# Kernel tuning notes

Measured on AMD Instinct MI355X. Metric: run time of the kernel, lower is better.

The kernel has to match this reference:

```python
import jax, jax.numpy as jnp
import numpy as np

Y = 1      # init kwarg y
DIM = 2    # init kwarg dim


def setup_inputs() -> dict:
    key = jax.random.key(0)
    k1, k2, k3 = jax.random.split(key, 3)
    B, L = 16, 512
    H = 32
    x = jax.random.normal(k1, (B, L, L), dtype=jnp.float32)
    # xavier_uniform-like init for weights
    lim1 = np.sqrt(6.0 / (3 + H)).astype(np.float32)
    W1 = jax.random.uniform(k2, (H, 3), dtype=jnp.float32, minval=-lim1, maxval=lim1)
    b1 = jnp.zeros((H,), dtype=jnp.float32)
    lim2 = np.sqrt(6.0 / (H + 1)).astype(np.float32)
    W2 = jax.random.uniform(k3, (1, H), dtype=jnp.float32, minval=-lim2, maxval=lim2)
    b2 = jnp.zeros((1,), dtype=jnp.float32)
    return {"x": x, "W1": W1, "b1": b1, "W2": W2, "b2": b2}


def reference(x, W1, b1, W2, b2):
    # nearest-neighbor sum along both lattice dims
    x1 = (jnp.roll(x, 1, axis=1) + jnp.roll(x, -1, axis=1)
          + jnp.roll(x, 1, axis=2) + jnp.roll(x, -1, axis=2))
    # shifted-by-y neighbor sum along DIM
    sx = jnp.roll(x, Y, axis=DIM) + jnp.roll(x, -Y, axis=DIM)
    # per-site 3-feature vector: [x^2, x1*x, sx*x] -> (B, L, L, 3)
    inp = jnp.stack([x * x, x1 * x, sx * x], axis=-1)
    # tiny pointwise MLP 3 -> 32 -> 1
    h = jnp.tanh(jnp.einsum('blmf,hf->blmh', inp, W1) + b1)
    out = jnp.einsum('blmh,oh->blmo', h, W2)[..., 0] + b2[0]
    # sum over lattice sites -> per-config scalar (B,)
    return out.sum(axis=(1, 2))
```

## Files before the change

### kernel.cpp

```cpp
#include <hip/hip_runtime.h>

#define L 512
#define LMASK 511
#define HID 32

constexpr int THREADS        = 256;
constexpr int ROWS_PER_BLOCK = 4;
constexpr int BLOCKS_PER_B   = L / ROWS_PER_BLOCK;
constexpr int NTAB           = 4096;
constexpr int GT             = 5;
constexpr int NPAIR_E        = 6;

constexpr float MAGIC = 8388608.0f;
constexpr float BIASB = 8194.0f;

__global__ __launch_bounds__(THREADS)
void site_kernel(const float* __restrict__ x,
                 const float* __restrict__ W1,
                 const float* __restrict__ b1,
                 const float* __restrict__ W2,
                 float* __restrict__ partial) {
    __shared__ __align__(16) float tab_s[NTAB];
    __shared__ __align__(16) float zw_s[GT * 16];
    __shared__ __align__(16) float w2t_s[GT * 4];
    __shared__ __align__(16) float ew_s[NPAIR_E * 8];
    __shared__ __align__(8)  float ew2_s[NPAIR_E * 2];

    const int t = threadIdx.x;
    const float Ke = 2.8853900817779268f;

    if (t < HID) {
        if (t < 4 * GT) {
            const float K256 = 256.0f * Ke;
            const int g = t >> 2, q = t & 3;
            zw_s[g * 16 +  0 + q] = K256 * W1[t * 3 + 0];
            zw_s[g * 16 +  4 + q] = K256 * W1[t * 3 + 1];
            zw_s[g * 16 +  8 + q] = K256 * W1[t * 3 + 2];
            zw_s[g * 16 + 12 + q] = fmaf(K256, b1[t], BIASB + MAGIC);
            w2t_s[t] = -2.0f * W2[t];
        } else {
            const int e = t - 4 * GT, p = e >> 1, q = e & 1;
            ew_s[p * 8 + 0 + q] = Ke * W1[t * 3 + 0];
            ew_s[p * 8 + 2 + q] = Ke * W1[t * 3 + 1];
            ew_s[p * 8 + 4 + q] = Ke * W1[t * 3 + 2];
            ew_s[p * 8 + 6 + q] = Ke * b1[t];
            ew2_s[p * 2 + q]    = -2.0f * W2[t];
        }
    }
    for (int i = t; i < NTAB; i += THREADS) {
        const float zp = fmaf((float)i, 0.015625f, -32.001953125f);
        tab_s[i] = __builtin_amdgcn_rcpf(1.0f + __builtin_amdgcn_exp2f(zp));
    }
    __syncthreads();

    const int blk = blockIdx.x;
    const int b   = blk >> 7;
    const int i0  = (blk & (BLOCKS_PER_B - 1)) * ROWS_PER_BLOCK;
    const float* __restrict__ xb = x + (size_t)b * (L * L);

    float F0[8], F1[8], F2[8];
#pragma unroll
    for (int g = 0; g < 2; ++g) {
        const int j  = t + g * THREADS;
        const int jm = (j + LMASK) & LMASK, jp = (j + 1) & LMASK;

        float cc[6];
#pragma unroll
        for (int r = 0; r < 6; ++r) {
            const int i = (i0 + r - 1 + L) & LMASK;
            cc[r] = xb[i * L + j];
        }
#pragma unroll
        for (int s = 0; s < 4; ++s) {
            const int i   = i0 + s;
            const float lf = xb[i * L + jm];
            const float rg = xb[i * L + jp];
            const float c  = cc[s + 1];
            const float lr = lf + rg;
            const float x1 = lr + cc[s] + cc[s + 2];
            const int k = g * 4 + s;
            F0[k] = c * c;  F1[k] = x1 * c;  F2[k] = lr * c;
        }
    }

    float acc[8] = {0.f, 0.f, 0.f, 0.f, 0.f, 0.f, 0.f, 0.f};
    const char* __restrict__ tb = (const char*)tab_s;

    auto tgroup = [&](const int gq) {
        const float4 wa  = *(const float4*)&zw_s[gq * 16 + 0];
        const float4 wb  = *(const float4*)&zw_s[gq * 16 + 4];
        const float4 wc  = *(const float4*)&zw_s[gq * 16 + 8];
        const float4 w0  = *(const float4*)&zw_s[gq * 16 + 12];
        const float4 w2v = *(const float4*)&w2t_s[gq * 4];
#pragma unroll
        for (int q = 0; q < 4; ++q) {
            const float waq = ((const float*)&wa)[q];
            const float wbq = ((const float*)&wb)[q];
            const float wcq = ((const float*)&wc)[q];
            const float w0q = ((const float*)&w0)[q];
            const float w2q = ((const float*)&w2v)[q];
#pragma unroll
            for (int s = 0; s < 8; ++s) {
                const float uu = fmaf(F0[s], waq, fmaf(F1[s], wbq, fmaf(F2[s], wcq, w0q)));
                const int  off = __float_as_int(uu) & 0x3FFC;
                const float y  = *reinterpret_cast<const float*>(tb + off);
                acc[s] = fmaf(w2q, y, acc[s]);
            }
        }
    };
    auto epair = [&](const int p) {
        const float4 e0 = *(const float4*)&ew_s[p * 8 + 0];
        const float4 e1 = *(const float4*)&ew_s[p * 8 + 4];
        const float2 w2p = *(const float2*)&ew2_s[p * 2];
        const float wa0 = e0.x, wa1 = e0.y, wb0 = e0.z, wb1 = e0.w;
        const float wc0 = e1.x, wc1 = e1.y, w00 = e1.z, w01 = e1.w;
#pragma unroll
        for (int s = 0; s < 8; ++s) {
            const float z0 = fmaf(F0[s], wa0, fmaf(F1[s], wb0, fmaf(F2[s], wc0, w00)));
            const float z1 = fmaf(F0[s], wa1, fmaf(F1[s], wb1, fmaf(F2[s], wc1, w01)));
            const float d0 = 1.0f + __builtin_amdgcn_exp2f(z0);
            const float d1 = 1.0f + __builtin_amdgcn_exp2f(z1);
            const float nm = fmaf(w2p.x, d1, w2p.y * d0);
            const float rr = __builtin_amdgcn_rcpf(d0 * d1);
            acc[s] = fmaf(nm, rr, acc[s]);
        }
    };

    tgroup(0); epair(0);
    tgroup(1); epair(1);
    tgroup(2); epair(2);
    tgroup(3); epair(3);
    tgroup(4); epair(4); epair(5);

    float a = ((acc[0] + acc[1]) + (acc[2] + acc[3]))
            + ((acc[4] + acc[5]) + (acc[6] + acc[7]));
#pragma unroll
    for (int off = 32; off > 0; off >>= 1)
        a += __shfl_down(a, off, 64);

    __shared__ float wsum[THREADS / 64];
    const int wid = t >> 6, lane = t & 63;
    if (lane == 0) wsum[wid] = a;
    __syncthreads();
    if (t == 0)
        partial[blk] = (wsum[0] + wsum[1]) + (wsum[2] + wsum[3]);
}

__global__ __launch_bounds__(128)
void reduce_kernel(const float* __restrict__ partial,
                   const float* __restrict__ W2,
                   const float* __restrict__ b2,
                   float* __restrict__ out) {
    const int b = blockIdx.x, t = threadIdx.x;
    const float NS = (float)(L * L);

    float v = partial[b * BLOCKS_PER_B + t];
    if (t < HID) v += NS * W2[t];
    if (t == 0)  v += NS * b2[0];

#pragma unroll
    for (int off = 32; off > 0; off >>= 1)
        v += __shfl_down(v, off, 64);

    __shared__ float ws2[2];
    if ((t & 63) == 0) ws2[t >> 6] = v;
    __syncthreads();
    if (t == 0) out[b] = ws2[0] + ws2[1];
}

extern "C" void kernel_launch(void* const* d_in, const int* in_sizes, int n_in,
                              void* d_out, int out_size, void* d_ws, size_t ws_size,
                              hipStream_t stream) {
    const float* x  = (const float*)d_in[0];
    const float* W1 = (const float*)d_in[1];
    const float* b1 = (const float*)d_in[2];
    const float* W2 = (const float*)d_in[3];
    const float* b2 = (const float*)d_in[4];
    float* out      = (float*)d_out;
    float* partial  = (float*)d_ws;

    const int B = in_sizes[0] / (L * L);

    site_kernel<<<B * BLOCKS_PER_B, THREADS, 0, stream>>>(x, W1, b1, W2, partial);
    reduce_kernel<<<B, 128, 0, stream>>>(partial, W2, b2, out);
}
```

Baseline: 34.15 us.

## Halve rows per block and split table lookups into address/load/consume phases

Each block now covers 2 rows instead of 4, which doubles the grid to 4096 blocks, and the reduce kernel is widened to 256 threads to match. The table-lookup path is split into three steps: compute all 16 LDS offsets, issue all 16 LDS loads, run the exp-based pair evaluation, then consume the loaded values. This interleaves LDS latency with transcendental work. In exchange, every block still builds the 4096-entry sigmoid table, so twice as many blocks repeat that setup, and halo rows are reloaded more often.

```diff
diff --git a/kernel.cpp b/kernel.cpp
--- a/kernel.cpp
+++ b/kernel.cpp
@@ -5,7 +5,7 @@
 #define HID 32
 
 constexpr int THREADS        = 256;
-constexpr int ROWS_PER_BLOCK = 4;
+constexpr int ROWS_PER_BLOCK = 2;
 constexpr int BLOCKS_PER_B   = L / ROWS_PER_BLOCK;
 constexpr int NTAB           = 4096;
 constexpr int GT             = 5;
@@ -54,86 +54,100 @@
     __syncthreads();
 
     const int blk = blockIdx.x;
-    const int b   = blk >> 7;
+    const int b   = blk >> 8;
     const int i0  = (blk & (BLOCKS_PER_B - 1)) * ROWS_PER_BLOCK;
     const float* __restrict__ xb = x + (size_t)b * (L * L);
 
-    float F0[8], F1[8], F2[8];
+    float F0[4], F1[4], F2[4];
 #pragma unroll
     for (int g = 0; g < 2; ++g) {
         const int j  = t + g * THREADS;
         const int jm = (j + LMASK) & LMASK, jp = (j + 1) & LMASK;
 
-        float cc[6];
-#pragma unroll
-        for (int r = 0; r < 6; ++r) {
+        float cc[4];
+#pragma unroll
+        for (int r = 0; r < 4; ++r) {
             const int i = (i0 + r - 1 + L) & LMASK;
             cc[r] = xb[i * L + j];
         }
 #pragma unroll
-        for (int s = 0; s < 4; ++s) {
+        for (int s = 0; s < 2; ++s) {
             const int i   = i0 + s;
             const float lf = xb[i * L + jm];
             const float rg = xb[i * L + jp];
             const float c  = cc[s + 1];
             const float lr = lf + rg;
             const float x1 = lr + cc[s] + cc[s + 2];
-            const int k = g * 4 + s;
+            const int k = g * 2 + s;
             F0[k] = c * c;  F1[k] = x1 * c;  F2[k] = lr * c;
         }
     }
 
-    float acc[8] = {0.f, 0.f, 0.f, 0.f, 0.f, 0.f, 0.f, 0.f};
+    float acc[4] = {0.f, 0.f, 0.f, 0.f};
     const char* __restrict__ tb = (const char*)tab_s;
 
-    auto tgroup = [&](const int gq) {
-        const float4 wa  = *(const float4*)&zw_s[gq * 16 + 0];
-        const float4 wb  = *(const float4*)&zw_s[gq * 16 + 4];
-        const float4 wc  = *(const float4*)&zw_s[gq * 16 + 8];
-        const float4 w0  = *(const float4*)&zw_s[gq * 16 + 12];
-        const float4 w2v = *(const float4*)&w2t_s[gq * 4];
+    int   offs[16];
+    float tt[16];
+
+    auto taddr = [&](const int gq) {
+        const float4 wa = *(const float4*)&zw_s[gq * 16 + 0];
+        const float4 wb = *(const float4*)&zw_s[gq * 16 + 4];
+        const float4 wc = *(const float4*)&zw_s[gq * 16 + 8];
+        const float4 w0 = *(const float4*)&zw_s[gq * 16 + 12];
 #pragma unroll
         for (int q = 0; q < 4; ++q) {
             const float waq = ((const float*)&wa)[q];
             const float wbq = ((const float*)&wb)[q];
             const float wcq = ((const float*)&wc)[q];
             const float w0q = ((const float*)&w0)[q];
+#pragma unroll
+            for (int s = 0; s < 4; ++s) {
+                const float uu = fmaf(F0[s], waq, fmaf(F1[s], wbq, fmaf(F2[s], wcq, w0q)));
+                offs[q * 4 + s] = __float_as_int(uu) & 0x3FFC;
+            }
+        }
+    };
+    auto tload = [&]() {
+#pragma unroll
+        for (int i = 0; i < 16; ++i)
+            tt[i] = *reinterpret_cast<const float*>(tb + offs[i]);
+    };
+    auto tcons = [&](const int gq) {
+        const float4 w2v = *(const float4*)&w2t_s[gq * 4];
+#pragma unroll
+        for (int q = 0; q < 4; ++q) {
             const float w2q = ((const float*)&w2v)[q];
 #pragma unroll
-            for (int s = 0; s < 8; ++s) {
-                const float uu = fmaf(F0[s], waq, fmaf(F1[s], wbq, fmaf(F2[s], wcq, w0q)));
-                const int  off = __float_as_int(uu) & 0x3FFC;
-                const float y  = *reinterpret_cast<const float*>(tb + off);
-                acc[s] = fmaf(w2q, y, acc[s]);
-            }
+            for (int s = 0; s < 4; ++s)
+                acc[s] = fmaf(w2q, tt[q * 4 + s], acc[s]);
         }
     };
     auto epair = [&](const int p) {
         const float4 e0 = *(const float4*)&ew_s[p * 8 + 0];
         const float4 e1 = *(const float4*)&ew_s[p * 8 + 4];
-        const float2 w2p = *(const float2*)&ew2_s[p * 2];
+        const float2 wp = *(const float2*)&ew2_s[p * 2];
         const float wa0 = e0.x, wa1 = e0.y, wb0 = e0.z, wb1 = e0.w;
         const float wc0 = e1.x, wc1 = e1.y, w00 = e1.z, w01 = e1.w;
 #pragma unroll
-        for (int s = 0; s < 8; ++s) {
+        for (int s = 0; s < 4; ++s) {
             const float z0 = fmaf(F0[s], wa0, fmaf(F1[s], wb0, fmaf(F2[s], wc0, w00)));
             const float z1 = fmaf(F0[s], wa1, fmaf(F1[s], wb1, fmaf(F2[s], wc1, w01)));
             const float d0 = 1.0f + __builtin_amdgcn_exp2f(z0);
             const float d1 = 1.0f + __builtin_amdgcn_exp2f(z1);
-            const float nm = fmaf(w2p.x, d1, w2p.y * d0);
+            const float nm = fmaf(wp.x, d1, wp.y * d0);
             const float rr = __builtin_amdgcn_rcpf(d0 * d1);
             acc[s] = fmaf(nm, rr, acc[s]);
         }
     };
 
-    tgroup(0); epair(0);
-    tgroup(1); epair(1);
-    tgroup(2); epair(2);
-    tgroup(3); epair(3);
-    tgroup(4); epair(4); epair(5);
-
-    float a = ((acc[0] + acc[1]) + (acc[2] + acc[3]))
-            + ((acc[4] + acc[5]) + (acc[6] + acc[7]));
+    taddr(0); tload(); epair(0); tcons(0);
+    taddr(1); tload(); epair(1); tcons(1);
+    taddr(2); tload(); epair(2); tcons(2);
+    taddr(3); tload(); epair(3); tcons(3);
+    taddr(4); tload(); epair(4); tcons(4);
+    epair(5);
+
+    float a = (acc[0] + acc[1]) + (acc[2] + acc[3]);
 #pragma unroll
     for (int off = 32; off > 0; off >>= 1)
         a += __shfl_down(a, off, 64);
@@ -146,7 +160,7 @@
         partial[blk] = (wsum[0] + wsum[1]) + (wsum[2] + wsum[3]);
 }
 
-__global__ __launch_bounds__(128)
+__global__ __launch_bounds__(256)
 void reduce_kernel(const float* __restrict__ partial,
                    const float* __restrict__ W2,
                    const float* __restrict__ b2,
@@ -162,10 +176,10 @@
     for (int off = 32; off > 0; off >>= 1)
         v += __shfl_down(v, off, 64);
 
-    __shared__ float ws2[2];
-    if ((t & 63) == 0) ws2[t >> 6] = v;
+    __shared__ float ws4[4];
+    if ((t & 63) == 0) ws4[t >> 6] = v;
     __syncthreads();
-    if (t == 0) out[b] = ws2[0] + ws2[1];
+    if (t == 0) out[b] = (ws4[0] + ws4[1]) + (ws4[2] + ws4[3]);
 }
 
 extern "C" void kernel_launch(void* const* d_in, const int* in_sizes, int n_in,
@@ -182,5 +196,5 @@
     const int B = in_sizes[0] / (L * L);
 
     site_kernel<<<B * BLOCKS_PER_B, THREADS, 0, stream>>>(x, W1, b1, W2, partial);
-    reduce_kernel<<<B, 128, 0, stream>>>(partial, W2, b2, out);
+    reduce_kernel<<<B, 256, 0, stream>>>(partial, W2, b2, out);
 }
```

Measured after the change: 33.77 us. No clear change (-1.1%).
